# Optimization experiments

Measured on AMD Instinct MI355X. Metric: run time of the kernel, lower is better.

Reference implementation:

```python
import jax, jax.numpy as jnp
import numpy as np

B, T, V, D = 128, 512, 8000, 256
H = D // 2   # per-direction LSTM hidden
L = 4        # label_dim


def setup_inputs() -> dict:
    key = jax.random.key(0)
    ks = jax.random.split(key, 16)
    s = 0.1
    pad_seq = jax.random.randint(ks[0], (B, T), 0, V)
    lens = jax.random.randint(ks[1], (B,), 1, T + 1)
    lens = lens.at[0].set(T)  # padded length == max(lens), as pad_packed_sequence would give
    emb = (jax.random.normal(ks[2], (V, D)) * s).at[0].set(0.0)  # padding_idx=0
    return {
        "pad_seq": pad_seq, "lens": lens, "emb": emb,
        "W_ih_f": jax.random.normal(ks[3], (4 * H, D)) * s,
        "W_hh_f": jax.random.normal(ks[4], (4 * H, H)) * s,
        "b_ih_f": jax.random.normal(ks[5], (4 * H,)) * s,
        "b_hh_f": jax.random.normal(ks[6], (4 * H,)) * s,
        "W_ih_b": jax.random.normal(ks[7], (4 * H, D)) * s,
        "W_hh_b": jax.random.normal(ks[8], (4 * H, H)) * s,
        "b_ih_b": jax.random.normal(ks[9], (4 * H,)) * s,
        "b_hh_b": jax.random.normal(ks[10], (4 * H,)) * s,
        "W_lab": jax.random.normal(ks[11], (L, D)) * s,
        "b_lab": jax.random.normal(ks[12], (L,)) * s,
        "transitions": jax.random.normal(ks[13], (L, L)),
        "from_BOS": jax.random.normal(ks[14], (L,)),
        "to_EOS": jax.random.normal(ks[15], (L,)),
    }


def _lstm(xs_t, mask_t, Wih, Whh, bih, bhh, reverse):
    """Masked unidirectional LSTM over time-major xs_t [T,B,D]; emulates
    pack_padded_sequence semantics (state frozen and output zeroed at pads)."""
    nb, nh = xs_t.shape[1], Whh.shape[1]

    def step(carry, inp):
        h, c = carry
        x_t, m_t = inp  # [B,D], [B,1] bool
        g = x_t @ Wih.T + bih + h @ Whh.T + bhh
        i, f, gg, o = jnp.split(g, 4, axis=-1)
        c2 = jax.nn.sigmoid(f) * c + jax.nn.sigmoid(i) * jnp.tanh(gg)
        h2 = jax.nn.sigmoid(o) * jnp.tanh(c2)
        h = jnp.where(m_t, h2, h)
        c = jnp.where(m_t, c2, c)
        return (h, c), jnp.where(m_t, h2, 0.0)

    init = (jnp.zeros((nb, nh), xs_t.dtype), jnp.zeros((nb, nh), xs_t.dtype))
    _, ys = jax.lax.scan(step, init, (xs_t, mask_t), reverse=reverse)
    return ys  # [T,B,H]


def reference(pad_seq, lens, emb, W_ih_f, W_hh_f, b_ih_f, b_hh_f,
              W_ih_b, W_hh_b, b_ih_b, b_hh_b, W_lab, b_lab,
              transitions, from_BOS, to_EOS):
    b, t = pad_seq.shape
    x = emb[pad_seq]                       # [B,T,D]
    xs_t = jnp.transpose(x, (1, 0, 2))     # [T,B,D]
    mask_t = (jnp.arange(t)[:, None] < lens[None, :])[:, :, None]  # [T,B,1]

    hf = _lstm(xs_t, mask_t, W_ih_f, W_hh_f, b_ih_f, b_hh_f, reverse=False)
    hb = _lstm(xs_t, mask_t, W_ih_b, W_hh_b, b_ih_b, b_hh_b, reverse=True)
    h = jnp.concatenate([hf, hb], axis=-1)           # [T,B,D]
    scores = h @ W_lab.T + b_lab                     # [T,B,L] emissions

    # --- Viterbi forward pass ---
    best0 = from_BOS[None, :] + scores[0]            # [B,L]

    def vstep(best, inp):
        ti, e = inp                                  # step index, emissions [B,L]
        smat = best[:, :, None] + e[:, None, :] + transitions[None]  # [B,prev,cur]
        valid = (lens > ti)[:, None]
        nb = jnp.where(valid, smat.max(axis=1), best)
        return nb, jnp.argmax(smat, axis=1)          # backtrace [B,L]

    bestT, bt = jax.lax.scan(vstep, best0, (jnp.arange(1, t), scores[1:]))
    final_vec = bestT + to_EOS[None, :]              # [B,L]
    last_lab = jnp.argmax(final_vec, axis=1)         # [B]

    # --- backtrace: label[t] = bt[t][label[t+1]] for t < len-1 ---
    bt_pad = jnp.concatenate([bt, jnp.zeros((1,) + bt.shape[1:], bt.dtype)], axis=0)  # [T,B,L]

    def bstep(cur, inp):
        ti, bt_t = inp
        cand = jnp.take_along_axis(bt_t, cur[:, None], axis=1)[:, 0]
        cur = jnp.where(ti == lens - 1, last_lab,
                        jnp.where(ti < lens - 1, cand, cur))
        return cur, cur

    _, labs = jax.lax.scan(bstep, jnp.zeros((b,), last_lab.dtype),
                           (jnp.arange(t), bt_pad), reverse=True)
    labels = labs.T  # [B,T]
    len_bool = jnp.arange(t)[None, :] < lens[:, None]
    return labels * len_bool
```

## Files before the change

### kernel.cpp

```cpp
#include <hip/hip_runtime.h>
#include <math.h>

#define VOCAB 8000
#define BATCH 128
#define TMAX  512
#define DIM   256
#define HID   128
#define G4    512
#define NCOL  1024

__device__ __forceinline__ float dpp_xor1(float x) {
  int r = __builtin_amdgcn_update_dpp(0, __builtin_bit_cast(int, x),
                                      0xB1, 0xF, 0xF, true);
  return __builtin_bit_cast(float, r);
}
__device__ __forceinline__ float dpp_xor2(float x) {
  int r = __builtin_amdgcn_update_dpp(0, __builtin_bit_cast(int, x),
                                      0x4E, 0xF, 0xF, true);
  return __builtin_bit_cast(float, r);
}
__device__ __forceinline__ unsigned dpp_xor1u(unsigned x) {
  return (unsigned)__builtin_amdgcn_update_dpp(0, (int)x, 0xB1, 0xF, 0xF, true);
}
__device__ __forceinline__ unsigned dpp_xor2u(unsigned x) {
  return (unsigned)__builtin_amdgcn_update_dpp(0, (int)x, 0x4E, 0xF, 0xF, true);
}
__device__ __forceinline__ float dpp_bc0(float x) {
  int r = __builtin_amdgcn_update_dpp(0, __builtin_bit_cast(int, x),
                                      0x00, 0xF, 0xF, true);
  return __builtin_bit_cast(float, r);
}
__device__ __forceinline__ float dpp_bc1(float x) {
  int r = __builtin_amdgcn_update_dpp(0, __builtin_bit_cast(int, x),
                                      0x55, 0xF, 0xF, true);
  return __builtin_bit_cast(float, r);
}
__device__ __forceinline__ float dpp_bc2(float x) {
  int r = __builtin_amdgcn_update_dpp(0, __builtin_bit_cast(int, x),
                                      0xAA, 0xF, 0xF, true);
  return __builtin_bit_cast(float, r);
}
__device__ __forceinline__ float dpp_bc3(float x) {
  int r = __builtin_amdgcn_update_dpp(0, __builtin_bit_cast(int, x),
                                      0xFF, 0xF, 0xF, true);
  return __builtin_bit_cast(float, r);
}

__global__ __launch_bounds__(256) void embw_gemm(
    const float* __restrict__ emb,
    const float* __restrict__ Wf, const float* __restrict__ Wb,
    const float* __restrict__ bihf, const float* __restrict__ bhhf,
    const float* __restrict__ bihb, const float* __restrict__ bhhb,
    float* __restrict__ embW) {
  __shared__ float As[32][132];
  __shared__ float Bs[32][132];
  const int tid = threadIdx.x;
  const int m0 = blockIdx.x * 128;
  const int n0 = blockIdx.y * 128;
  const int tx = tid & 15, ty = tid >> 4;
  const int lrow = tid >> 1;
  const int lseg = (tid & 1) * 16;
  const float* Wsrc = (n0 < 512) ? Wf : Wb;
  const int nbase = (n0 < 512) ? n0 : (n0 - 512);

  float acc[8][8];
  #pragma unroll
  for (int i = 0; i < 8; ++i)
    #pragma unroll
    for (int jj = 0; jj < 8; ++jj) acc[i][jj] = 0.f;

  for (int k0 = 0; k0 < 256; k0 += 32) {
    const int gm = m0 + lrow;
    #pragma unroll
    for (int q = 0; q < 4; ++q) {
      float4 v = make_float4(0.f, 0.f, 0.f, 0.f);
      if (gm < VOCAB) v = *(const float4*)(emb + (size_t)gm * 256 + k0 + lseg + 4 * q);
      As[lseg + 4*q + 0][lrow] = v.x;
      As[lseg + 4*q + 1][lrow] = v.y;
      As[lseg + 4*q + 2][lrow] = v.z;
      As[lseg + 4*q + 3][lrow] = v.w;
    }
    #pragma unroll
    for (int q = 0; q < 4; ++q) {
      float4 v = *(const float4*)(Wsrc + (size_t)(nbase + lrow) * 256 + k0 + lseg + 4 * q);
      Bs[lseg + 4*q + 0][lrow] = v.x;
      Bs[lseg + 4*q + 1][lrow] = v.y;
      Bs[lseg + 4*q + 2][lrow] = v.z;
      Bs[lseg + 4*q + 3][lrow] = v.w;
    }
    __syncthreads();
    #pragma unroll
    for (int k = 0; k < 32; ++k) {
      float4 av0 = *(const float4*)&As[k][ty * 8];
      float4 av1 = *(const float4*)&As[k][ty * 8 + 4];
      float4 bv0 = *(const float4*)&Bs[k][tx * 4];
      float4 bv1 = *(const float4*)&Bs[k][64 + tx * 4];
      float a[8]  = {av0.x, av0.y, av0.z, av0.w, av1.x, av1.y, av1.z, av1.w};
      float bb[8] = {bv0.x, bv0.y, bv0.z, bv0.w, bv1.x, bv1.y, bv1.z, bv1.w};
      #pragma unroll
      for (int i = 0; i < 8; ++i)
        #pragma unroll
        for (int jj = 0; jj < 8; ++jj)
          acc[i][jj] += a[i] * bb[jj];
    }
    __syncthreads();
  }

  float bias[8];
  #pragma unroll
  for (int jj = 0; jj < 8; ++jj) {
    int n = n0 + ((jj < 4) ? (tx * 4 + jj) : (64 + tx * 4 + (jj - 4)));
    bias[jj] = (n < 512) ? (bihf[n] + bhhf[n]) : (bihb[n - 512] + bhhb[n - 512]);
  }
  #pragma unroll
  for (int i = 0; i < 8; ++i) {
    int gm = m0 + ty * 8 + i;
    if (gm >= VOCAB) continue;
    float4 v0 = make_float4(acc[i][0] + bias[0], acc[i][1] + bias[1],
                            acc[i][2] + bias[2], acc[i][3] + bias[3]);
    float4 v1 = make_float4(acc[i][4] + bias[4], acc[i][5] + bias[5],
                            acc[i][6] + bias[6], acc[i][7] + bias[7]);
    *(float4*)(embW + (size_t)gm * NCOL + n0 + tx * 4) = v0;
    *(float4*)(embW + (size_t)gm * NCOL + n0 + 64 + tx * 4) = v1;
  }
}

#define REP8(M) M(0) M(1) M(2) M(3) M(4) M(5) M(6) M(7)
#define REP8G(M,G) M(G,0) M(G,1) M(G,2) M(G,3) M(G,4) M(G,5) M(G,6) M(G,7)

__global__ __launch_bounds__(512)
__attribute__((amdgpu_waves_per_eu(2, 2)))
void lstm_rec(
    const int* __restrict__ pad_seq, const int* __restrict__ lens,
    const float* __restrict__ Whh_f, const float* __restrict__ Whh_b,
    const float* __restrict__ embW, const float* __restrict__ W_lab,
    float* __restrict__ e_part) {
  const int dir = blockIdx.x & 1;
  const int b   = blockIdx.x >> 1;
  const int tid = threadIdx.x;
  const int j   = tid >> 2;
  const int q   = tid & 3;
  const int parity = q & 1;
  const int half   = (q >> 1) & 1;

  __shared__ float ring[8][4][36];
  __shared__ float wls[4][132];
  __shared__ int   tok[TMAX];

  tok[tid] = pad_seq[b * TMAX + tid];
  wls[tid >> 7][tid & 127] = W_lab[(tid >> 7) * DIM + dir * HID + (tid & 127)];
  if (tid < 144) ((float*)ring)[tid] = 0.f;

  const int len = lens[b];
  const float* __restrict__ Whh = dir ? Whh_b : Whh_f;

  const float4* wr0 = (const float4*)(Whh + (size_t)(0 * HID + j) * HID + 32 * q);
  const float4* wr1 = (const float4*)(Whh + (size_t)(1 * HID + j) * HID + 32 * q);
  const float4* wr2 = (const float4*)(Whh + (size_t)(2 * HID + j) * HID + 32 * q);
  const float4* wr3 = (const float4*)(Whh + (size_t)(3 * HID + j) * HID + 32 * q);
#define DECLW(G,I)                                                      \
  float w##G##_##I##_0, w##G##_##I##_1, w##G##_##I##_2, w##G##_##I##_3; \
  { float4 t = wr##G[I];                                                \
    w##G##_##I##_0 = t.x; w##G##_##I##_1 = t.y;                         \
    w##G##_##I##_2 = t.z; w##G##_##I##_3 = t.w; }                       \
  asm volatile("" : "+v"(w##G##_##I##_0));                              \
  asm volatile("" : "+v"(w##G##_##I##_1));                              \
  asm volatile("" : "+v"(w##G##_##I##_2));                              \
  asm volatile("" : "+v"(w##G##_##I##_3));
  REP8G(DECLW,0) REP8G(DECLW,1) REP8G(DECLW,2) REP8G(DECLW,3)
#undef DECLW

  float c = 0.f;
  const float ascale = (q == 2) ? 2.f : 1.f;
  const float* __restrict__ ecol = embW + dir * G4 + (q * HID + j);
  float* __restrict__ ep = e_part + (size_t)(dir * BATCH + b) * TMAX * 4;

  __syncthreads();

  float xb0, xb1, xb2, xb3, xb4, xb5, xb6, xb7;
#define PRE(r) { const int ss = nbase + r; xb##r = 0.f;                 \
    if (ss < len) {                                                     \
      const int tt = dir ? (len - 1 - ss) : ss;                         \
      xb##r = ecol[(size_t)tok[tt] * NCOL]; } }
  { const int nbase = 0; REP8(PRE) }

#define MACC(G,I)                                         \
    a##G##0 = fmaf(hv##I.x, w##G##_##I##_0, a##G##0);     \
    a##G##1 = fmaf(hv##I.y, w##G##_##I##_1, a##G##1);     \
    a##G##2 = fmaf(hv##I.z, w##G##_##I##_2, a##G##2);     \
    a##G##3 = fmaf(hv##I.w, w##G##_##I##_3, a##G##3);

#define STEP(r, XW)                                                     \
  {                                                                     \
    const float4* h4 = (const float4*)&ring[r][q][0];                   \
    float4 hv0 = h4[0], hv1 = h4[1], hv2 = h4[2], hv3 = h4[3];          \
    float4 hv4 = h4[4], hv5 = h4[5], hv6 = h4[6], hv7 = h4[7];          \
    float a00=0.f,a01=0.f,a02=0.f,a03=0.f;                              \
    float a10=0.f,a11=0.f,a12=0.f,a13=0.f;                              \
    float a20=0.f,a21=0.f,a22=0.f,a23=0.f;                              \
    float a30=0.f,a31=0.f,a32=0.f,a33=0.f;                              \
    REP8G(MACC,0) REP8G(MACC,1) REP8G(MACC,2) REP8G(MACC,3)             \
    const float p0 = (a00+a01)+(a02+a03);                               \
    const float p1 = (a10+a11)+(a12+a13);                               \
    const float p2 = (a20+a21)+(a22+a23);                               \
    const float p3 = (a30+a31)+(a32+a33);                               \
     \
    const float klo = parity ? p1 : p0, slo = parity ? p0 : p1;         \
    const float khi = parity ? p3 : p2, shi = parity ? p2 : p3;         \
    const float alo = klo + dpp_xor1(slo);                              \
    const float ahi = khi + dpp_xor1(shi);                              \
    const float kb = half ? ahi : alo, sb = half ? alo : ahi;           \
    const float tot = kb + dpp_xor2(sb);                                \
    const float aa = tot + (XW);                                        \
    const float sg = 1.f / (1.f + __expf(-ascale * aa));                \
    const float act = (q == 2) ? (2.f * sg - 1.f) : sg;                 \
                          \
    const float e1 = dpp_xor1(act);                                     \
    const float e2 = dpp_xor2(act);                                     \
    const float e3 = dpp_xor2(e1);                                      \
    const float ev  = parity ? e1 : act, od  = parity ? act : e1;       \
    const float ev2 = parity ? e3 : e2,  od2 = parity ? e2 : e3;        \
    const float ig = half ? ev2 : ev, fg = half ? od2 : od;             \
    const float gt = half ? ev : ev2, og = half ? od : od2;             \
    c = fg * c + ig * gt;                                               \
    const float s2 = 1.f / (1.f + __expf(-2.f * c));                    \
    const float hh = og * (2.f * s2 - 1.f);                             \
    if (q == 0) ring[(r + 1) & 7][j >> 5][j & 31] = hh;                 \
    __syncthreads();                                                    \
  }

  for (int s0 = 0; s0 < len; s0 += 8) {
    const int cnt = (len - s0 < 8) ? (len - s0) : 8;
    STEP(0, xb0)
    if (cnt > 1) STEP(1, xb1)
    if (cnt > 2) STEP(2, xb2)
    if (cnt > 3) STEP(3, xb3)
    if (cnt > 4) STEP(4, xb4)
    if (cnt > 5) STEP(5, xb5)
    if (cnt > 6) STEP(6, xb6)
    if (cnt > 7) STEP(7, xb7)
    { const int nbase = s0 + 8; REP8(PRE) }
    {
      const int r = tid >> 6, l = (tid >> 4) & 3, sub = tid & 15;
      if (r < cnt) {
        const float4* hp = (const float4*)&ring[(r + 1) & 7][sub >> 2][8 * (sub & 3)];
        const float4 h0 = hp[0], h1 = hp[1];
        const float4* wp = (const float4*)&wls[l][8 * sub];
        const float4 u0 = wp[0], u1 = wp[1];
        float d = h0.x*u0.x + h0.y*u0.y + h0.z*u0.z + h0.w*u0.w
                + h1.x*u1.x + h1.y*u1.y + h1.z*u1.z + h1.w*u1.w;
        d += __shfl_xor(d, 1); d += __shfl_xor(d, 2);
        d += __shfl_xor(d, 4); d += __shfl_xor(d, 8);
        if (sub == 0) {
          const int ss = s0 + r;
          const int tt = dir ? (len - 1 - ss) : ss;
          ep[tt * 4 + l] = d;
        }
      }
    }
    asm volatile("" : "+v"(xb0), "+v"(xb1), "+v"(xb2), "+v"(xb3),
                      "+v"(xb4), "+v"(xb5), "+v"(xb6), "+v"(xb7));
    __syncthreads();
  }
#undef STEP
#undef MACC
#undef PRE
}

__global__ __launch_bounds__(512) void viterbi_k(
    const int* __restrict__ lens, const float* __restrict__ e_part,
    const float* __restrict__ b_lab, const float* __restrict__ trans,
    const float* __restrict__ from_BOS, const float* __restrict__ to_EOS,
    int* __restrict__ out) {
  const int b = blockIdx.x;
  const int tid = threadIdx.x;
  __shared__ float sc[TMAX][4];
  __shared__ unsigned btm[TMAX];
  __shared__ int labs[TMAX];
  const int len = lens[b];

  if (tid < len) {
    const float4 f  = *(const float4*)(e_part + ((size_t)b * TMAX + tid) * 4);
    const float4 g2 = *(const float4*)(e_part + ((size_t)(BATCH + b) * TMAX + tid) * 4);
    const float4 bl = *(const float4*)b_lab;
    sc[tid][0] = f.x + g2.x + bl.x;
    sc[tid][1] = f.y + g2.y + bl.y;
    sc[tid][2] = f.z + g2.z + bl.z;
    sc[tid][3] = f.w + g2.w + bl.w;
  }
  __syncthreads();

  if (tid < 4) {
    const int l = tid;
    float trc0 = trans[0 * 4 + l], trc1 = trans[1 * 4 + l];
    float trc2 = trans[2 * 4 + l], trc3 = trans[3 * 4 + l];
    float best = from_BOS[l] + sc[0][l];
    float e_next = sc[1][l];
    for (int ti = 1; ti < len; ++ti) {
      const float e = e_next;
      e_next = sc[(ti + 1 < TMAX) ? ti + 1 : ti][l];
      const float b0 = dpp_bc0(best);
      const float b1 = dpp_bc1(best);
      const float b2 = dpp_bc2(best);
      const float b3 = dpp_bc3(best);
      float m = (b0 + e) + trc0; int arg = 0;
      float v;
      v = (b1 + e) + trc1; if (v > m) { m = v; arg = 1; }
      v = (b2 + e) + trc2; if (v > m) { m = v; arg = 2; }
      v = (b3 + e) + trc3; if (v > m) { m = v; arg = 3; }
      best = m;
      unsigned av = ((unsigned)arg) << (8 * l);
      av |= dpp_xor1u(av);
      av |= dpp_xor2u(av);
      if (l == 0) btm[ti] = av;
    }
    const float f0 = dpp_bc0(best) + to_EOS[0];
    const float f1 = dpp_bc1(best) + to_EOS[1];
    const float f2 = dpp_bc2(best) + to_EOS[2];
    const float f3 = dpp_bc3(best) + to_EOS[3];
    if (l == 0) {
      float m = f0; int last = 0;
      if (f1 > m) { m = f1; last = 1; }
      if (f2 > m) { m = f2; last = 2; }
      if (f3 > m) { m = f3; last = 3; }
      labs[len - 1] = last;
      int cur = last;
      #pragma unroll 4
      for (int ti = len - 2; ti >= 0; --ti) {
        cur = (int)((btm[ti + 1] >> (8 * cur)) & 255u);
        labs[ti] = cur;
      }
    }
  }
  __syncthreads();
  out[b * TMAX + tid] = (tid < len) ? labs[tid] : 0;
}

extern "C" void kernel_launch(void* const* d_in, const int* in_sizes, int n_in,
                              void* d_out, int out_size, void* d_ws, size_t ws_size,
                              hipStream_t stream) {
  const int*   pad_seq  = (const int*)d_in[0];
  const int*   lens     = (const int*)d_in[1];
  const float* emb      = (const float*)d_in[2];
  const float* W_ih_f   = (const float*)d_in[3];
  const float* W_hh_f   = (const float*)d_in[4];
  const float* b_ih_f   = (const float*)d_in[5];
  const float* b_hh_f   = (const float*)d_in[6];
  const float* W_ih_b   = (const float*)d_in[7];
  const float* W_hh_b   = (const float*)d_in[8];
  const float* b_ih_b   = (const float*)d_in[9];
  const float* b_hh_b   = (const float*)d_in[10];
  const float* W_lab    = (const float*)d_in[11];
  const float* b_lab    = (const float*)d_in[12];
  const float* trans    = (const float*)d_in[13];
  const float* from_BOS = (const float*)d_in[14];
  const float* to_EOS   = (const float*)d_in[15];
  int* out = (int*)d_out;

  float* embW   = (float*)d_ws;
  float* e_part = embW + (size_t)VOCAB * NCOL;

  embw_gemm<<<dim3(63, 8), 256, 0, stream>>>(emb, W_ih_f, W_ih_b,
                                             b_ih_f, b_hh_f, b_ih_b, b_hh_b, embW);
  lstm_rec<<<dim3(2 * BATCH), 512, 0, stream>>>(pad_seq, lens, W_hh_f, W_hh_b,
                                                embW, W_lab, e_part);
  viterbi_k<<<dim3(BATCH), 512, 0, stream>>>(lens, e_part, b_lab, trans,
                                             from_BOS, to_EOS, out);
}
```

Measured before the change: 581.7 us.

## Prefetch global tiles, LDS-only barriers, earlier token prefetch, batched Viterbi loads

Result: no change. 585.9 us (+0.7%).

```diff
diff --git a/kernel.cpp b/kernel.cpp
--- a/kernel.cpp
+++ b/kernel.cpp
@@ -8,6 +8,8 @@
 #define HID   128
 #define G4    512
 #define NCOL  1024
+
+#define BARLDS() asm volatile("s_waitcnt lgkmcnt(0)\n\ts_barrier" ::: "memory")
 
 __device__ __forceinline__ float dpp_xor1(float x) {
   int r = __builtin_amdgcn_update_dpp(0, __builtin_bit_cast(int, x),
@@ -62,6 +64,7 @@
   const int lseg = (tid & 1) * 16;
   const float* Wsrc = (n0 < 512) ? Wf : Wb;
   const int nbase = (n0 < 512) ? n0 : (n0 - 512);
+  const int gm = m0 + lrow;
 
   float acc[8][8];
   #pragma unroll
@@ -69,26 +72,31 @@
     #pragma unroll
     for (int jj = 0; jj < 8; ++jj) acc[i][jj] = 0.f;
 
+  float4 la[4], lb[4];
+#define LOADT(K0)                                                         \
+  { _Pragma("unroll")                                                     \
+    for (int qq = 0; qq < 4; ++qq) {                                      \
+      la[qq] = make_float4(0.f, 0.f, 0.f, 0.f);                           \
+      if (gm < VOCAB)                                                     \
+        la[qq] = *(const float4*)(emb + (size_t)gm * 256 + (K0) + lseg + 4 * qq); \
+      lb[qq] = *(const float4*)(Wsrc + (size_t)(nbase + lrow) * 256 + (K0) + lseg + 4 * qq); \
+    } }
+
+  LOADT(0)
   for (int k0 = 0; k0 < 256; k0 += 32) {
-    const int gm = m0 + lrow;
     #pragma unroll
-    for (int q = 0; q < 4; ++q) {
-      float4 v = make_float4(0.f, 0.f, 0.f, 0.f);
-      if (gm < VOCAB) v = *(const float4*)(emb + (size_t)gm * 256 + k0 + lseg + 4 * q);
-      As[lseg + 4*q + 0][lrow] = v.x;
-      As[lseg + 4*q + 1][lrow] = v.y;
-      As[lseg + 4*q + 2][lrow] = v.z;
-      As[lseg + 4*q + 3][lrow] = v.w;
-    }
-    #pragma unroll
-    for (int q = 0; q < 4; ++q) {
-      float4 v = *(const float4*)(Wsrc + (size_t)(nbase + lrow) * 256 + k0 + lseg + 4 * q);
-      Bs[lseg + 4*q + 0][lrow] = v.x;
-      Bs[lseg + 4*q + 1][lrow] = v.y;
-      Bs[lseg + 4*q + 2][lrow] = v.z;
-      Bs[lseg + 4*q + 3][lrow] = v.w;
+    for (int qq = 0; qq < 4; ++qq) {
+      As[lseg + 4*qq + 0][lrow] = la[qq].x;
+      As[lseg + 4*qq + 1][lrow] = la[qq].y;
+      As[lseg + 4*qq + 2][lrow] = la[qq].z;
+      As[lseg + 4*qq + 3][lrow] = la[qq].w;
+      Bs[lseg + 4*qq + 0][lrow] = lb[qq].x;
+      Bs[lseg + 4*qq + 1][lrow] = lb[qq].y;
+      Bs[lseg + 4*qq + 2][lrow] = lb[qq].z;
+      Bs[lseg + 4*qq + 3][lrow] = lb[qq].w;
     }
     __syncthreads();
+    if (k0 + 32 < 256) LOADT(k0 + 32)
     #pragma unroll
     for (int k = 0; k < 32; ++k) {
       float4 av0 = *(const float4*)&As[k][ty * 8];
@@ -105,6 +113,7 @@
     }
     __syncthreads();
   }
+#undef LOADT
 
   float bias[8];
   #pragma unroll
@@ -114,14 +123,14 @@
   }
   #pragma unroll
   for (int i = 0; i < 8; ++i) {
-    int gm = m0 + ty * 8 + i;
-    if (gm >= VOCAB) continue;
+    int gmo = m0 + ty * 8 + i;
+    if (gmo >= VOCAB) continue;
     float4 v0 = make_float4(acc[i][0] + bias[0], acc[i][1] + bias[1],
                             acc[i][2] + bias[2], acc[i][3] + bias[3]);
     float4 v1 = make_float4(acc[i][4] + bias[4], acc[i][5] + bias[5],
                             acc[i][6] + bias[6], acc[i][7] + bias[7]);
-    *(float4*)(embW + (size_t)gm * NCOL + n0 + tx * 4) = v0;
-    *(float4*)(embW + (size_t)gm * NCOL + n0 + 64 + tx * 4) = v1;
+    *(float4*)(embW + (size_t)gmo * NCOL + n0 + tx * 4) = v0;
+    *(float4*)(embW + (size_t)gmo * NCOL + n0 + 64 + tx * 4) = v1;
   }
 }
 
@@ -178,11 +187,17 @@
   __syncthreads();
 
   float xb0, xb1, xb2, xb3, xb4, xb5, xb6, xb7;
-#define PRE(r) { const int ss = nbase + r; xb##r = 0.f;                 \
+  float yb0, yb1, yb2, yb3, yb4, yb5, yb6, yb7;
+#define PREX(r) { const int ss = r; xb##r = 0.f;                        \
     if (ss < len) {                                                     \
       const int tt = dir ? (len - 1 - ss) : ss;                         \
       xb##r = ecol[(size_t)tok[tt] * NCOL]; } }
-  { const int nbase = 0; REP8(PRE) }
+  REP8(PREX)
+#undef PREX
+#define PREY(r) { const int ss = nbase + r; yb##r = 0.f;                \
+    if (ss < len) {                                                     \
+      const int tt = dir ? (len - 1 - ss) : ss;                         \
+      yb##r = ecol[(size_t)tok[tt] * NCOL]; } }
 
 #define MACC(G,I)                                         \
     a##G##0 = fmaf(hv##I.x, w##G##_##I##_0, a##G##0);     \
@@ -204,7 +219,6 @@
     const float p1 = (a10+a11)+(a12+a13);                               \
     const float p2 = (a20+a21)+(a22+a23);                               \
     const float p3 = (a30+a31)+(a32+a33);                               \
-     \
     const float klo = parity ? p1 : p0, slo = parity ? p0 : p1;         \
     const float khi = parity ? p3 : p2, shi = parity ? p2 : p3;         \
     const float alo = klo + dpp_xor1(slo);                              \
@@ -214,7 +228,6 @@
     const float aa = tot + (XW);                                        \
     const float sg = 1.f / (1.f + __expf(-ascale * aa));                \
     const float act = (q == 2) ? (2.f * sg - 1.f) : sg;                 \
-                          \
     const float e1 = dpp_xor1(act);                                     \
     const float e2 = dpp_xor2(act);                                     \
     const float e3 = dpp_xor2(e1);                                      \
@@ -226,7 +239,7 @@
     const float s2 = 1.f / (1.f + __expf(-2.f * c));                    \
     const float hh = og * (2.f * s2 - 1.f);                             \
     if (q == 0) ring[(r + 1) & 7][j >> 5][j & 31] = hh;                 \
-    __syncthreads();                                                    \
+    BARLDS();                                                           \
   }
 
   for (int s0 = 0; s0 < len; s0 += 8) {
@@ -235,11 +248,11 @@
     if (cnt > 1) STEP(1, xb1)
     if (cnt > 2) STEP(2, xb2)
     if (cnt > 3) STEP(3, xb3)
+    { const int nbase = s0 + 8; REP8(PREY) }
     if (cnt > 4) STEP(4, xb4)
     if (cnt > 5) STEP(5, xb5)
     if (cnt > 6) STEP(6, xb6)
     if (cnt > 7) STEP(7, xb7)
-    { const int nbase = s0 + 8; REP8(PRE) }
     {
       const int r = tid >> 6, l = (tid >> 4) & 3, sub = tid & 15;
       if (r < cnt) {
@@ -258,13 +271,13 @@
         }
       }
     }
-    asm volatile("" : "+v"(xb0), "+v"(xb1), "+v"(xb2), "+v"(xb3),
-                      "+v"(xb4), "+v"(xb5), "+v"(xb6), "+v"(xb7));
-    __syncthreads();
+    BARLDS();
+    xb0 = yb0; xb1 = yb1; xb2 = yb2; xb3 = yb3;
+    xb4 = yb4; xb5 = yb5; xb6 = yb6; xb7 = yb7;
   }
 #undef STEP
 #undef MACC
-#undef PRE
+#undef PREY
 }
 
 __global__ __launch_bounds__(512) void viterbi_k(
@@ -295,10 +308,14 @@
     float trc0 = trans[0 * 4 + l], trc1 = trans[1 * 4 + l];
     float trc2 = trans[2 * 4 + l], trc3 = trans[3 * 4 + l];
     float best = from_BOS[l] + sc[0][l];
-    float e_next = sc[1][l];
+    float eA = sc[(1 < TMAX) ? 1 : 0][l];
+    float eB = sc[(2 < TMAX) ? 2 : 0][l];
+    float eC = sc[(3 < TMAX) ? 3 : 0][l];
     for (int ti = 1; ti < len; ++ti) {
-      const float e = e_next;
-      e_next = sc[(ti + 1 < TMAX) ? ti + 1 : ti][l];
+      const float e = eA;
+      eA = eB; eB = eC;
+      int nx = ti + 3; if (nx > TMAX - 1) nx = TMAX - 1;
+      eC = sc[nx][l];
       const float b0 = dpp_bc0(best);
       const float b1 = dpp_bc1(best);
       const float b2 = dpp_bc2(best);
@@ -325,10 +342,25 @@
       if (f3 > m) { m = f3; last = 3; }
       labs[len - 1] = last;
       int cur = last;
-      #pragma unroll 4
-      for (int ti = len - 2; ti >= 0; --ti) {
-        cur = (int)((btm[ti + 1] >> (8 * cur)) & 255u);
-        labs[ti] = cur;
+      int ti = len - 2;
+      while (ti >= 0) {
+        const int hi = ti + 1;
+        const unsigned u0 = btm[hi];
+        const unsigned u1 = (hi - 1 >= 1) ? btm[hi - 1] : 0u;
+        const unsigned u2 = (hi - 2 >= 1) ? btm[hi - 2] : 0u;
+        const unsigned u3 = (hi - 3 >= 1) ? btm[hi - 3] : 0u;
+        const unsigned u4 = (hi - 4 >= 1) ? btm[hi - 4] : 0u;
+        const unsigned u5 = (hi - 5 >= 1) ? btm[hi - 5] : 0u;
+        const unsigned u6 = (hi - 6 >= 1) ? btm[hi - 6] : 0u;
+        const unsigned u7 = (hi - 7 >= 1) ? btm[hi - 7] : 0u;
+        cur = (int)((u0 >> (8 * cur)) & 255u); labs[ti--] = cur; if (ti < 0) break;
+        cur = (int)((u1 >> (8 * cur)) & 255u); labs[ti--] = cur; if (ti < 0) break;
+        cur = (int)((u2 >> (8 * cur)) & 255u); labs[ti--] = cur; if (ti < 0) break;
+        cur = (int)((u3 >> (8 * cur)) & 255u); labs[ti--] = cur; if (ti < 0) break;
+        cur = (int)((u4 >> (8 * cur)) & 255u); labs[ti--] = cur; if (ti < 0) break;
+        cur = (int)((u5 >> (8 * cur)) & 255u); labs[ti--] = cur; if (ti < 0) break;
+        cur = (int)((u6 >> (8 * cur)) & 255u); labs[ti--] = cur; if (ti < 0) break;
+        cur = (int)((u7 >> (8 * cur)) & 255u); labs[ti--] = cur;
       }
     }
   }
```
